# Performance work log

Measured on AMD Instinct MI355X. Metric: run time of the kernel, lower is better.

## Reference

```python
import jax, jax.numpy as jnp
import numpy as np

B, L, D, H, NB = 32, 200, 512, 8, 2
HD = D // H
EPS = 1e-8


def _ln(x, g, b):
    m = x.mean(-1, keepdims=True)
    v = ((x - m) ** 2).mean(-1, keepdims=True)
    return (x - m) / jnp.sqrt(v + EPS) * g + b


def setup_inputs() -> dict:
    key = jax.random.key(0)
    ks = jax.random.split(key, 12)
    w = lambda k, shape: (jax.random.normal(k, shape, jnp.float32) * 0.02)
    return {
        "x": jax.random.normal(ks[0], (B, L, D), jnp.float32),
        "timeline_mask": jnp.zeros((B, L), dtype=bool),  # True = padded
        "ln1_g": jnp.ones((NB, D), jnp.float32), "ln1_b": jnp.zeros((NB, D), jnp.float32),
        "Wq": w(ks[1], (NB, D, D)), "bq": jnp.zeros((NB, D), jnp.float32),
        "Wk": w(ks[2], (NB, D, D)), "bk": jnp.zeros((NB, D), jnp.float32),
        "Wv": w(ks[3], (NB, D, D)), "bv": jnp.zeros((NB, D), jnp.float32),
        "Wo": w(ks[4], (NB, D, D)), "bo": jnp.zeros((NB, D), jnp.float32),
        "ln2_g": jnp.ones((NB, D), jnp.float32), "ln2_b": jnp.zeros((NB, D), jnp.float32),
        "W1": w(ks[5], (NB, D, D)), "b1": jnp.zeros((NB, D), jnp.float32),
        "W2": w(ks[6], (NB, D, D)), "b2": jnp.zeros((NB, D), jnp.float32),
        "lnf_g": jnp.ones((D,), jnp.float32), "lnf_b": jnp.zeros((D,), jnp.float32),
    }


def reference(x, timeline_mask, ln1_g, ln1_b, Wq, bq, Wk, bk, Wv, bv, Wo, bo,
              ln2_g, ln2_b, W1, b1, W2, b2, lnf_g, lnf_b):
    valid = (~timeline_mask)[..., None].astype(x.dtype)  # [B,L,1]
    # causal additive bias [L,L]: 0 on/below diag, -inf above
    causal = jnp.where(jnp.tril(jnp.ones((L, L), dtype=bool)), 0.0, -jnp.inf).astype(x.dtype)
    scale = 1.0 / (HD ** 0.5)
    q = x * valid  # dropout = identity (eval)
    for i in range(NB):
        Qn = _ln(q, ln1_g[i], ln1_b[i])  # pre-attn LayerNorm (query side)
        qh = (Qn @ Wq[i] + bq[i]).reshape(B, L, H, HD)
        kh = (q @ Wk[i] + bk[i]).reshape(B, L, H, HD)
        vh = (q @ Wv[i] + bv[i]).reshape(B, L, H, HD)
        scores = jnp.einsum('bqhd,bkhd->bhqk', qh, kh) * scale + causal
        attn = jax.nn.softmax(scores, axis=-1)
        ctx = jnp.einsum('bhqk,bkhd->bqhd', attn, vh).reshape(B, L, D)
        q = ctx @ Wo[i] + bo[i] + Qn          # residual to normed Q (as in source)
        q = _ln(q, ln2_g[i], ln2_b[i])        # forward layernorm
        h = jax.nn.relu(q @ W1[i] + b1[i]) @ W2[i] + b2[i]  # 1x1 convs == per-token MLP
        q = (q + h) * valid                   # PWFF residual, then timeline mask
    return _ln(q, lnf_g, lnf_b)
```

## Files before the change

kernel.cpp:

```cpp
#include <hip/hip_runtime.h>

typedef unsigned short u16;
typedef __bf16 bfloat;
typedef bfloat bf16x8 __attribute__((ext_vector_type(8)));
typedef float f32x4 __attribute__((ext_vector_type(4)));
typedef u16 v8u16 __attribute__((ext_vector_type(8)));
typedef u16 v4u16 __attribute__((ext_vector_type(4)));

#define B_ 32
#define L_ 200
#define D_ 512
#define H_ 8
#define HD_ 64
#define M_ (B_*L_)

__device__ __forceinline__ float bf2f(u16 u) {
  union { float f; unsigned int i; } v; v.i = ((unsigned int)u) << 16; return v.f;
}
__device__ __forceinline__ u16 f2bf(float f) {
  union { float f; unsigned int i; } v; v.f = f;
  unsigned int i = v.i;
  return (u16)((i + 0x7FFFu + ((i >> 16) & 1u)) >> 16);
}
__device__ __forceinline__ bf16x8 as_bf(v8u16 v) { return __builtin_bit_cast(bf16x8, v); }

__device__ __forceinline__ void gload16(const void* g, void* l) {
  __builtin_amdgcn_global_load_lds(
      (const __attribute__((address_space(1))) void*)g,
      (__attribute__((address_space(3))) void*)l,
      16, 0, 0);
}

struct TPtrs { const float* s[12]; };

__global__ __launch_bounds__(256) void prep_kernel(
    const float* __restrict__ x, const unsigned char* __restrict__ mask,
    u16* __restrict__ qb, TPtrs tp, u16* __restrict__ dst,
    const float* __restrict__ ln1g, const float* __restrict__ ln1b, u16* __restrict__ Qn)
{
  __shared__ float T[64][65];
  int bid = blockIdx.x;
  int t = threadIdx.x;
  if (bid < 1600) {
    size_t i = (size_t)bid * 256 + t;
    size_t base = i * 8;
    int tok = (int)(base >> 9);
    float valid = mask[tok] ? 0.f : 1.f;
    float4 v0 = *(const float4*)(x + base);
    float4 v1 = *(const float4*)(x + base + 4);
    v8u16 ob;
    ob[0]=f2bf(v0.x*valid); ob[1]=f2bf(v0.y*valid); ob[2]=f2bf(v0.z*valid); ob[3]=f2bf(v0.w*valid);
    ob[4]=f2bf(v1.x*valid); ob[5]=f2bf(v1.y*valid); ob[6]=f2bf(v1.z*valid); ob[7]=f2bf(v1.w*valid);
    *(v8u16*)(qb + base) = ob;
    int lane = t & 63;
    float xs[8];
    #pragma unroll
    for (int j = 0; j < 8; j++) xs[j] = bf2f(ob[j]);
    float s = 0.f, q = 0.f;
    #pragma unroll
    for (int j = 0; j < 8; j++) { s += xs[j]; q += xs[j] * xs[j]; }
    #pragma unroll
    for (int off = 1; off < 64; off <<= 1) { s += __shfl_xor(s, off); q += __shfl_xor(q, off); }
    float mean = s * (1.f / 512.f);
    float var  = fmaxf(q * (1.f / 512.f) - mean * mean, 0.f);
    float rstd = rsqrtf(var + 1e-8f);
    float4 g0 = *(const float4*)(ln1g + lane * 8);
    float4 g1 = *(const float4*)(ln1g + lane * 8 + 4);
    float4 b0 = *(const float4*)(ln1b + lane * 8);
    float4 b1 = *(const float4*)(ln1b + lane * 8 + 4);
    float gv[8] = {g0.x,g0.y,g0.z,g0.w,g1.x,g1.y,g1.z,g1.w};
    float bv[8] = {b0.x,b0.y,b0.z,b0.w,b1.x,b1.y,b1.z,b1.w};
    v8u16 qn;
    #pragma unroll
    for (int j = 0; j < 8; j++) qn[j] = f2bf((xs[j] - mean) * rstd * gv[j] + bv[j]);
    *(v8u16*)(Qn + base) = qn;
  } else {
    int wb   = bid - 1600;
    int mat  = wb >> 6;
    int tile = wb & 63;
    int tr = tile >> 3, tc = tile & 7;
    const float* src = tp.s[mat];
    #pragma unroll
    for (int i = 0; i < 4; i++) {
      int idx = t + i * 256;
      int row = idx >> 4, c4 = idx & 15;
      float4 v = *(const float4*)(src + (size_t)(tr * 64 + row) * 512 + tc * 64 + c4 * 4);
      T[row][c4 * 4 + 0] = v.x; T[row][c4 * 4 + 1] = v.y;
      T[row][c4 * 4 + 2] = v.z; T[row][c4 * 4 + 3] = v.w;
    }
    __syncthreads();
    u16* d = dst + (size_t)mat * 262144;
    #pragma unroll
    for (int i = 0; i < 2; i++) {
      int idx = t + i * 256;
      int row = idx >> 3, c8 = idx & 7;
      v8u16 v;
      #pragma unroll
      for (int j = 0; j < 8; j++) v[j] = f2bf(T[c8 * 8 + j][row]);
      *(v8u16*)(d + (size_t)(tc * 64 + row) * 512 + tr * 64 + c8 * 8) = v;
    }
  }
}

template<bool OUTF32>
__global__ __launch_bounds__(256) void ln_kernel(
    const u16* __restrict__ in, const float* __restrict__ g, const float* __restrict__ b,
    u16* __restrict__ outb, float* __restrict__ outf)
{
  int row  = blockIdx.x * 4 + (threadIdx.x >> 6);
  int lane = threadIdx.x & 63;
  size_t base = (size_t)row * 512 + lane * 8;
  v8u16 xv = *(const v8u16*)(in + base);
  float xs[8];
  #pragma unroll
  for (int j = 0; j < 8; j++) xs[j] = bf2f(xv[j]);
  float s = 0.f, q = 0.f;
  #pragma unroll
  for (int j = 0; j < 8; j++) { s += xs[j]; q += xs[j] * xs[j]; }
  #pragma unroll
  for (int off = 1; off < 64; off <<= 1) { s += __shfl_xor(s, off); q += __shfl_xor(q, off); }
  float mean = s * (1.f / 512.f);
  float var  = fmaxf(q * (1.f / 512.f) - mean * mean, 0.f);
  float rstd = rsqrtf(var + 1e-8f);
  float4 g0 = *(const float4*)(g + lane * 8);
  float4 g1 = *(const float4*)(g + lane * 8 + 4);
  float4 b0 = *(const float4*)(b + lane * 8);
  float4 b1 = *(const float4*)(b + lane * 8 + 4);
  float gv[8] = {g0.x,g0.y,g0.z,g0.w,g1.x,g1.y,g1.z,g1.w};
  float bv[8] = {b0.x,b0.y,b0.z,b0.w,b1.x,b1.y,b1.z,b1.w};
  if (OUTF32) {
    float of[8];
    #pragma unroll
    for (int j = 0; j < 8; j++) of[j] = (xs[j] - mean) * rstd * gv[j] + bv[j];
    *(float4*)(outf + base)     = make_float4(of[0], of[1], of[2], of[3]);
    *(float4*)(outf + base + 4) = make_float4(of[4], of[5], of[6], of[7]);
  } else {
    v8u16 ob;
    #pragma unroll
    for (int j = 0; j < 8; j++) ob[j] = f2bf((xs[j] - mean) * rstd * gv[j] + bv[j]);
    *(v8u16*)(outb + base) = ob;
  }
}

__device__ __forceinline__ void stage128(const u16* __restrict__ src, int r0, int kk,
                                         u16* dstLds, int wid, int lane) {
  int g = lane & 15;
  #pragma unroll
  for (int j = 0; j < 4; j++) {
    int row = j * 16 + wid * 4 + (lane >> 4);
    int gsrc = (g & 8) | ((g & 7) ^ (row & 7));
    gload16(src + (size_t)(r0 + row) * 512 + kk + gsrc * 8,
            (char*)dstLds + (j * 16 + wid * 4) * 256);
  }
}

__device__ __forceinline__ void gemm_core128(
    const u16* __restrict__ A, const u16* __restrict__ Wt,
    int m0, int n0, u16* As, u16* Bs, f32x4 (&acc)[2][2])
{
  int tid = threadIdx.x, wid = tid >> 6, lane = tid & 63;
  int wr = wid >> 1, wc = wid & 1;
  int l15 = lane & 15, hi = lane >> 4;

  for (int s = 0; s < 4; s++) {
    int kk = s * 128;
    stage128(A,  m0, kk, As, wid, lane);
    stage128(Wt, n0, kk, Bs, wid, lane);
    __syncthreads();
    #pragma unroll
    for (int ksub = 0; ksub < 4; ksub++) {
      int G = ksub * 4 + hi;
      bf16x8 af[2], bfr[2];
      #pragma unroll
      for (int mi = 0; mi < 2; mi++) {
        int ra = wr * 32 + mi * 16 + l15;
        int lg = (G & 8) | ((G & 7) ^ (ra & 7));
        af[mi] = *(const bf16x8*)(As + ra * 128 + lg * 8);
      }
      #pragma unroll
      for (int ni = 0; ni < 2; ni++) {
        int rn = wc * 32 + ni * 16 + l15;
        int lg = (G & 8) | ((G & 7) ^ (rn & 7));
        bfr[ni] = *(const bf16x8*)(Bs + rn * 128 + lg * 8);
      }
      #pragma unroll
      for (int mi = 0; mi < 2; mi++)
        #pragma unroll
        for (int ni = 0; ni < 2; ni++)
          acc[mi][ni] = __builtin_amdgcn_mfma_f32_16x16x32_bf16(af[mi], bfr[ni], acc[mi][ni], 0, 0, 0);
    }
    __syncthreads();
  }
}

__device__ __forceinline__ void gemm_core128x64(
    const u16* __restrict__ A, const u16* __restrict__ Wt,
    int m0, int n0, u16* As, u16* Bs, f32x4 (&acc)[2][4])
{
  int tid = threadIdx.x, wid = tid >> 6, lane = tid & 63;
  int l15 = lane & 15, hi = lane >> 4;

  for (int s = 0; s < 4; s++) {
    int kk = s * 128;
    stage128(A,  m0,      kk, As,             wid, lane);
    stage128(A,  m0 + 64, kk, As + 64 * 128,  wid, lane);
    stage128(Wt, n0,      kk, Bs,             wid, lane);
    __syncthreads();
    #pragma unroll
    for (int ksub = 0; ksub < 4; ksub++) {
      int G = ksub * 4 + hi;
      bf16x8 af[2], bfr[4];
      #pragma unroll
      for (int mi = 0; mi < 2; mi++) {
        int ra = wid * 32 + mi * 16 + l15;
        int lg = (G & 8) | ((G & 7) ^ (ra & 7));
        af[mi] = *(const bf16x8*)(As + ra * 128 + lg * 8);
      }
      #pragma unroll
      for (int ni = 0; ni < 4; ni++) {
        int rn = ni * 16 + l15;
        int lg = (G & 8) | ((G & 7) ^ (rn & 7));
        bfr[ni] = *(const bf16x8*)(Bs + rn * 128 + lg * 8);
      }
      #pragma unroll
      for (int mi = 0; mi < 2; mi++)
        #pragma unroll
        for (int ni = 0; ni < 4; ni++)
          acc[mi][ni] = __builtin_amdgcn_mfma_f32_16x16x32_bf16(af[mi], bfr[ni], acc[mi][ni], 0, 0, 0);
    }
    __syncthreads();
  }
}

__device__ __forceinline__ void swz400t(int bid, int& m0, int& n0) {
  int tile = (bid & 7) * 50 + (bid >> 3);
  m0 = (tile >> 3) * 128;
  n0 = (tile & 7) * 64;
}

template<bool RELU, bool HAS_RES, bool MASK>
__global__ __launch_bounds__(256) void gemm_one(
    const u16* __restrict__ A, const u16* __restrict__ Wt, const float* __restrict__ bias,
    const u16* __restrict__ res, const unsigned char* __restrict__ mask,
    u16* __restrict__ outb)
{
  __shared__ u16 As[128 * 128];
  __shared__ u16 Bs[64 * 128];
  int m0, n0;
  swz400t(blockIdx.x, m0, n0);
  f32x4 acc[2][4] = {};
  gemm_core128x64(A, Wt, m0, n0, As, Bs, acc);

  int tid = threadIdx.x, wid = tid >> 6, lane = tid & 63;
  int l15 = lane & 15, hi = lane >> 4;
  #pragma unroll
  for (int ni = 0; ni < 4; ni++) {
    int gc = n0 + ni * 16 + l15;
    float bvv = bias[gc];
    #pragma unroll
    for (int mi = 0; mi < 2; mi++) {
      int grb = m0 + wid * 32 + mi * 16 + hi * 4;
      #pragma unroll
      for (int r = 0; r < 4; r++) {
        int gr = grb + r;
        float v = acc[mi][ni][r] + bvv;
        if (HAS_RES) v += bf2f(res[(size_t)gr * 512 + gc]);
        if (RELU) v = fmaxf(v, 0.f);
        if (MASK) v = mask[gr] ? 0.f : v;
        outb[(size_t)gr * 512 + gc] = f2bf(v);
      }
    }
  }
}

__global__ __launch_bounds__(256) void gemm_qkv(
    const u16* __restrict__ Aq, const u16* __restrict__ Akv,
    const u16* __restrict__ Wtq, const u16* __restrict__ Wtk, const u16* __restrict__ Wtv,
    const float* __restrict__ bq, const float* __restrict__ bk, const float* __restrict__ bv,
    u16* __restrict__ outq, u16* __restrict__ outk, u16* __restrict__ outvt)
{
  __shared__ u16 sh[3 * 64 * 128];
  int bid = blockIdx.x;
  int tile = (bid & 7) * 200 + (bid >> 3);
  int tid = threadIdx.x, wid = tid >> 6, lane = tid & 63;
  int wr = wid >> 1, wc = wid & 1;
  int l15 = lane & 15, hi = lane >> 4;
  u16* As = sh;
  u16* B0 = sh + 8192;
  u16* B1 = sh + 16384;

  if (tile < 800) {
    int m0 = (tile >> 3) * 64, n0 = (tile & 7) * 64;
    f32x4 acc[2][2] = {};
    gemm_core128(Aq, Wtq, m0, n0, As, B0, acc);
    #pragma unroll
    for (int ni = 0; ni < 2; ni++) {
      int gc = n0 + wc * 32 + ni * 16 + l15;
      float bvv = bq[gc];
      #pragma unroll
      for (int mi = 0; mi < 2; mi++) {
        int grb = m0 + wr * 32 + mi * 16 + hi * 4;
        #pragma unroll
        for (int r = 0; r < 4; r++)
          outq[(size_t)(grb + r) * 512 + gc] = f2bf(acc[mi][ni][r] + bvv);
      }
    }
  } else {
    int t2 = tile - 800;
    int m0 = (t2 >> 3) * 64, n0 = (t2 & 7) * 64;
    f32x4 ak[2][2] = {}, av[2][2] = {};
    for (int s = 0; s < 4; s++) {
      int kk = s * 128;
      stage128(Akv, m0, kk, As, wid, lane);
      stage128(Wtk, n0, kk, B0, wid, lane);
      stage128(Wtv, n0, kk, B1, wid, lane);
      __syncthreads();
      #pragma unroll
      for (int ksub = 0; ksub < 4; ksub++) {
        int G = ksub * 4 + hi;
        bf16x8 af[2], bkf[2], bvf[2];
        #pragma unroll
        for (int mi = 0; mi < 2; mi++) {
          int ra = wr * 32 + mi * 16 + l15;
          int lg = (G & 8) | ((G & 7) ^ (ra & 7));
          af[mi] = *(const bf16x8*)(As + ra * 128 + lg * 8);
        }
        #pragma unroll
        for (int ni = 0; ni < 2; ni++) {
          int rn = wc * 32 + ni * 16 + l15;
          int lg = (G & 8) | ((G & 7) ^ (rn & 7));
          bkf[ni] = *(const bf16x8*)(B0 + rn * 128 + lg * 8);
          bvf[ni] = *(const bf16x8*)(B1 + rn * 128 + lg * 8);
        }
        #pragma unroll
        for (int mi = 0; mi < 2; mi++)
          #pragma unroll
          for (int ni = 0; ni < 2; ni++) {
            ak[mi][ni] = __builtin_amdgcn_mfma_f32_16x16x32_bf16(af[mi], bkf[ni], ak[mi][ni], 0, 0, 0);
            av[mi][ni] = __builtin_amdgcn_mfma_f32_16x16x32_bf16(af[mi], bvf[ni], av[mi][ni], 0, 0, 0);
          }
      }
      __syncthreads();
    }
    #pragma unroll
    for (int ni = 0; ni < 2; ni++) {
      int gc = n0 + wc * 32 + ni * 16 + l15;
      float bkv = bk[gc], bvv = bv[gc];
      int h = gc >> 6, hd = gc & 63;
      #pragma unroll
      for (int mi = 0; mi < 2; mi++) {
        int grb = m0 + wr * 32 + mi * 16 + hi * 4;
        #pragma unroll
        for (int r = 0; r < 4; r++) {
          int gr = grb + r;
          outk[(size_t)gr * 512 + gc] = f2bf(ak[mi][ni][r] + bkv);
          int b = gr / 200, l = gr - b * 200;
          outvt[((size_t)(b * 8 + h) * 64 + hd) * 224 + l] = f2bf(av[mi][ni][r] + bvv);
        }
      }
    }
  }
}

__global__ __launch_bounds__(64) void attn_kernel(
    const u16* __restrict__ Qh, const u16* __restrict__ Kh,
    const u16* __restrict__ Vt, u16* __restrict__ ctx)
{
  __shared__ u16 Pb[2][16 * 32];
  int bid = blockIdx.x;
  int xcd = bid & 7, j = bid >> 3;
  int bh_hi = j / 7, s = j - bh_hi * 7;
  int bh = bh_hi * 8 + xcd;
  int b = bh >> 3, h = bh & 7;
  int lane = threadIdx.x;
  int l15 = lane & 15, hi = lane >> 4;

  const u16* Kg = Kh + (size_t)(b * L_) * D_ + h * HD_;
  const u16* Vg = Vt + (size_t)bh * 64 * 224;

  int tA = (s < 6) ? (12 - s) : 6;
  int tB = (s < 6) ? s : -1;

  for (int jj = 0; jj < 2; jj++) {
    int t = jj ? tB : tA;
    if (t < 0) break;
    int q0 = t * 16;
    int qrow = q0 + l15; if (qrow > L_ - 1) qrow = L_ - 1;
    const u16* Qg = Qh + (size_t)(b * L_ + qrow) * D_ + h * HD_ + hi * 8;
    bf16x8 aq0 = as_bf(*(const v8u16*)(Qg));
    bf16x8 aq1 = as_bf(*(const v8u16*)(Qg + 32));

    f32x4 sv[13];
    float m0[4];
    #pragma unroll
    for (int r = 0; r < 4; r++) m0[r] = -3.0e38f;

    #pragma unroll
    for (int kt = 0; kt < 13; kt++) {
      if (kt <= t) {
        const u16* kp = Kg + (size_t)(kt * 16 + l15) * D_ + hi * 8;
        bf16x8 bk0 = as_bf(*(const v8u16*)(kp));
        bf16x8 bk1 = as_bf(*(const v8u16*)(kp + 32));
        f32x4 a = {0.f, 0.f, 0.f, 0.f};
        a = __builtin_amdgcn_mfma_f32_16x16x32_bf16(aq0, bk0, a, 0, 0, 0);
        a = __builtin_amdgcn_mfma_f32_16x16x32_bf16(aq1, bk1, a, 0, 0, 0);
        #pragma unroll
        for (int r = 0; r < 4; r++) {
          int qr = q0 + hi * 4 + r;
          int kc = kt * 16 + l15;
          float val = (kc <= qr && qr < L_) ? a[r] * 0.125f : -3.0e38f;
          sv[kt][r] = val;
          m0[r] = fmaxf(m0[r], val);
        }
      }
    }
    #pragma unroll
    for (int r = 0; r < 4; r++) {
      #pragma unroll
      for (int off = 1; off < 16; off <<= 1)
        m0[r] = fmaxf(m0[r], __shfl_xor(m0[r], off));
      if (m0[r] < -1e37f) m0[r] = 0.f;
    }
    float sum[4] = {0.f, 0.f, 0.f, 0.f};
    #pragma unroll
    for (int kt = 0; kt < 13; kt++) {
      if (kt <= t) {
        #pragma unroll
        for (int r = 0; r < 4; r++) {
          float p = __expf(sv[kt][r] - m0[r]);
          sv[kt][r] = p;
          sum[r] += p;
        }
      }
    }
    #pragma unroll
    for (int r = 0; r < 4; r++) {
      #pragma unroll
      for (int off = 1; off < 16; off <<= 1) sum[r] += __shfl_xor(sum[r], off);
    }
    float inv[4];
    #pragma unroll
    for (int r = 0; r < 4; r++) inv[r] = sum[r] > 0.f ? 1.f / sum[r] : 0.f;

    int ksmax = (t + 2) >> 1;
    f32x4 acc[4] = {};
    #pragma unroll
    for (int ks = 0; ks < 7; ks++) {
      if (ks < ksmax) {
        u16* Ps = (u16*)Pb[ks & 1];
        #pragma unroll
        for (int half = 0; half < 2; half++) {
          int kt = ks * 2 + half;
          #pragma unroll
          for (int r = 0; r < 4; r++) {
            float pv = (kt <= t) ? sv[kt][r] : 0.f;
            Ps[(hi * 4 + r) * 32 + half * 16 + l15] = f2bf(pv);
          }
        }
        bf16x8 ap = as_bf(*(const v8u16*)(Ps + l15 * 32 + hi * 8));
        #pragma unroll
        for (int nt = 0; nt < 4; nt++) {
          bf16x8 bv = as_bf(*(const v8u16*)(Vg + (nt * 16 + l15) * 224 + ks * 32 + hi * 8));
          acc[nt] = __builtin_amdgcn_mfma_f32_16x16x32_bf16(ap, bv, acc[nt], 0, 0, 0);
        }
      }
    }
    #pragma unroll
    for (int nt = 0; nt < 4; nt++) {
      #pragma unroll
      for (int r = 0; r < 4; r++) {
        int qr = q0 + hi * 4 + r;
        if (qr < L_) ctx[(size_t)(b * L_ + qr) * D_ + h * HD_ + nt * 16 + l15] = f2bf(acc[nt][r] * inv[r]);
      }
    }
  }
}

extern "C" void kernel_launch(void* const* d_in, const int* in_sizes, int n_in,
                              void* d_out, int out_size, void* d_ws, size_t ws_size,
                              hipStream_t stream)
{
  (void)in_sizes; (void)n_in; (void)out_size; (void)ws_size;
  const float* x    = (const float*)d_in[0];
  const unsigned char* mask = (const unsigned char*)d_in[1];
  const float* ln1g = (const float*)d_in[2];
  const float* ln1b = (const float*)d_in[3];
  const float* Wq   = (const float*)d_in[4];
  const float* bq   = (const float*)d_in[5];
  const float* Wk   = (const float*)d_in[6];
  const float* bk   = (const float*)d_in[7];
  const float* Wv   = (const float*)d_in[8];
  const float* bv   = (const float*)d_in[9];
  const float* Wo   = (const float*)d_in[10];
  const float* bo   = (const float*)d_in[11];
  const float* ln2g = (const float*)d_in[12];
  const float* ln2b = (const float*)d_in[13];
  const float* W1   = (const float*)d_in[14];
  const float* b1   = (const float*)d_in[15];
  const float* W2   = (const float*)d_in[16];
  const float* b2   = (const float*)d_in[17];
  const float* lnfg = (const float*)d_in[18];
  const float* lnfb = (const float*)d_in[19];

  char* ws = (char*)d_ws;
  u16* Wt  = (u16*)(ws);
  u16* qb  = (u16*)(ws +  6291456);
  u16* Qn  = (u16*)(ws + 12845056);
  u16* qh  = (u16*)(ws + 19398656);
  u16* kh  = (u16*)(ws + 25952256);
  u16* vh  = (u16*)(ws + 32505856);
  u16* Vtb = (u16*)(ws + 39059456);

  TPtrs tp;
  tp.s[0] = Wq; tp.s[1] = Wq + 262144;
  tp.s[2] = Wk; tp.s[3] = Wk + 262144;
  tp.s[4] = Wv; tp.s[5] = Wv + 262144;
  tp.s[6] = Wo; tp.s[7] = Wo + 262144;
  tp.s[8] = W1; tp.s[9] = W1 + 262144;
  tp.s[10] = W2; tp.s[11] = W2 + 262144;

  prep_kernel<<<dim3(2368), dim3(256), 0, stream>>>(x, mask, qb, tp, Wt, ln1g, ln1b, Qn);

  for (int i = 0; i < 2; i++) {
    const u16* Wtq = Wt + (size_t)(0 + i) * 262144;
    const u16* Wtk = Wt + (size_t)(2 + i) * 262144;
    const u16* Wtv = Wt + (size_t)(4 + i) * 262144;
    const u16* Wto = Wt + (size_t)(6 + i) * 262144;
    const u16* Wt1 = Wt + (size_t)(8 + i) * 262144;
    const u16* Wt2 = Wt + (size_t)(10 + i) * 262144;

    if (i) ln_kernel<false><<<dim3(1600), dim3(256), 0, stream>>>(qb, ln1g + i * 512, ln1b + i * 512, Qn, nullptr);
    gemm_qkv<<<dim3(1600), dim3(256), 0, stream>>>(Qn, qb, Wtq, Wtk, Wtv,
                                                   bq + i * 512, bk + i * 512, bv + i * 512,
                                                   qh, kh, Vtb);
    attn_kernel<<<dim3(1792), dim3(64), 0, stream>>>(qh, kh, Vtb, vh);
    gemm_one<false,true,false><<<dim3(400), dim3(256), 0, stream>>>(vh, Wto, bo + i * 512, Qn, nullptr, qb);
    ln_kernel<false><<<dim3(1600), dim3(256), 0, stream>>>(qb, ln2g + i * 512, ln2b + i * 512, Qn, nullptr);
    gemm_one<true,false,false><<<dim3(400), dim3(256), 0, stream>>>(Qn, Wt1, b1 + i * 512, nullptr, nullptr, qh);
    gemm_one<false,true,true><<<dim3(400), dim3(256), 0, stream>>>(qh, Wt2, b2 + i * 512, Qn, mask, qb);
  }
  ln_kernel<true><<<dim3(1600), dim3(256), 0, stream>>>(qb, lnfg, lnfb, nullptr, (float*)d_out);
}
```

Baseline: 176.5 us.

## Fuse all stages into one persistent cooperative kernel with grid syncs

Replaces the chain of about 15 separate kernel launches with a single persistent cooperative kernel. It loops over work items per stage and separates stages with grid-wide barriers, removing launch overhead and inter-kernel gaps. The grid is capped at 512 workgroups, so large stages run several items per workgroup. Attention now packs four single-wave items into each 256-thread block. If the cooperative launch fails, it falls back to the old multi-kernel path.

Measured after the change: 205.0 us. 16.1% more time.

```diff
diff --git a/kernel.cpp b/kernel.cpp
--- a/kernel.cpp
+++ b/kernel.cpp
@@ -1,11 +1,13 @@
 #include <hip/hip_runtime.h>
+#include <hip/hip_cooperative_groups.h>
+
+namespace cg = cooperative_groups;
 
 typedef unsigned short u16;
 typedef __bf16 bfloat;
 typedef bfloat bf16x8 __attribute__((ext_vector_type(8)));
 typedef float f32x4 __attribute__((ext_vector_type(4)));
 typedef u16 v8u16 __attribute__((ext_vector_type(8)));
-typedef u16 v4u16 __attribute__((ext_vector_type(4)));
 
 #define B_ 32
 #define L_ 200
@@ -33,14 +35,12 @@
 
 struct TPtrs { const float* s[12]; };
 
-__global__ __launch_bounds__(256) void prep_kernel(
-    const float* __restrict__ x, const unsigned char* __restrict__ mask,
-    u16* __restrict__ qb, TPtrs tp, u16* __restrict__ dst,
-    const float* __restrict__ ln1g, const float* __restrict__ ln1b, u16* __restrict__ Qn)
-{
-  __shared__ float T[64][65];
-  int bid = blockIdx.x;
-  int t = threadIdx.x;
+
+__device__ void prep_item(const float* __restrict__ x, const unsigned char* __restrict__ mask,
+                          u16* __restrict__ qb, TPtrs tp, u16* __restrict__ Wt,
+                          const float* __restrict__ ln1g, const float* __restrict__ ln1b,
+                          u16* __restrict__ Qn, int bid, int t, float* T)
+{
   if (bid < 1600) {
     size_t i = (size_t)bid * 256 + t;
     size_t base = i * 8;
@@ -85,30 +85,29 @@
       int idx = t + i * 256;
       int row = idx >> 4, c4 = idx & 15;
       float4 v = *(const float4*)(src + (size_t)(tr * 64 + row) * 512 + tc * 64 + c4 * 4);
-      T[row][c4 * 4 + 0] = v.x; T[row][c4 * 4 + 1] = v.y;
-      T[row][c4 * 4 + 2] = v.z; T[row][c4 * 4 + 3] = v.w;
+      T[row * 65 + c4 * 4 + 0] = v.x; T[row * 65 + c4 * 4 + 1] = v.y;
+      T[row * 65 + c4 * 4 + 2] = v.z; T[row * 65 + c4 * 4 + 3] = v.w;
     }
     __syncthreads();
-    u16* d = dst + (size_t)mat * 262144;
+    u16* d = Wt + (size_t)mat * 262144;
     #pragma unroll
     for (int i = 0; i < 2; i++) {
       int idx = t + i * 256;
       int row = idx >> 3, c8 = idx & 7;
       v8u16 v;
       #pragma unroll
-      for (int j = 0; j < 8; j++) v[j] = f2bf(T[c8 * 8 + j][row]);
+      for (int j = 0; j < 8; j++) v[j] = f2bf(T[(c8 * 8 + j) * 65 + row]);
       *(v8u16*)(d + (size_t)(tc * 64 + row) * 512 + tr * 64 + c8 * 8) = v;
     }
   }
 }
 
 template<bool OUTF32>
-__global__ __launch_bounds__(256) void ln_kernel(
-    const u16* __restrict__ in, const float* __restrict__ g, const float* __restrict__ b,
-    u16* __restrict__ outb, float* __restrict__ outf)
-{
-  int row  = blockIdx.x * 4 + (threadIdx.x >> 6);
-  int lane = threadIdx.x & 63;
+__device__ void ln_item(int bid, int t, const u16* __restrict__ in,
+                        const float* __restrict__ g, const float* __restrict__ b,
+                        u16* __restrict__ outb, float* __restrict__ outf) {
+  int row  = bid * 4 + (t >> 6);
+  int lane = t & 63;
   size_t base = (size_t)row * 512 + lane * 8;
   v8u16 xv = *(const v8u16*)(in + base);
   float xs[8];
@@ -156,12 +155,11 @@
 
 __device__ __forceinline__ void gemm_core128(
     const u16* __restrict__ A, const u16* __restrict__ Wt,
-    int m0, int n0, u16* As, u16* Bs, f32x4 (&acc)[2][2])
-{
-  int tid = threadIdx.x, wid = tid >> 6, lane = tid & 63;
+    int m0, int n0, u16* As, u16* Bs, f32x4 (&acc)[2][2], int tid)
+{
+  int wid = tid >> 6, lane = tid & 63;
   int wr = wid >> 1, wc = wid & 1;
   int l15 = lane & 15, hi = lane >> 4;
-
   for (int s = 0; s < 4; s++) {
     int kk = s * 128;
     stage128(A,  m0, kk, As, wid, lane);
@@ -193,18 +191,24 @@
   }
 }
 
-__device__ __forceinline__ void gemm_core128x64(
-    const u16* __restrict__ A, const u16* __restrict__ Wt,
-    int m0, int n0, u16* As, u16* Bs, f32x4 (&acc)[2][4])
-{
-  int tid = threadIdx.x, wid = tid >> 6, lane = tid & 63;
+template<bool RELU, bool HAS_RES, bool MASK>
+__device__ void gemm_item(const u16* __restrict__ A, const u16* __restrict__ Wt,
+                          const float* __restrict__ bias, const u16* __restrict__ res,
+                          const unsigned char* __restrict__ mask, u16* __restrict__ outb,
+                          int bid, int tid, u16* sh)
+{
+  u16* As = sh;
+  u16* Bs = sh + 16384;
+  int tile = (bid & 7) * 50 + (bid >> 3);
+  int m0 = (tile >> 3) * 128, n0 = (tile & 7) * 64;
+  int wid = tid >> 6, lane = tid & 63;
   int l15 = lane & 15, hi = lane >> 4;
-
+  f32x4 acc[2][4] = {};
   for (int s = 0; s < 4; s++) {
     int kk = s * 128;
-    stage128(A,  m0,      kk, As,             wid, lane);
-    stage128(A,  m0 + 64, kk, As + 64 * 128,  wid, lane);
-    stage128(Wt, n0,      kk, Bs,             wid, lane);
+    stage128(A,  m0,      kk, As,            wid, lane);
+    stage128(A,  m0 + 64, kk, As + 64 * 128, wid, lane);
+    stage128(Wt, n0,      kk, Bs,            wid, lane);
     __syncthreads();
     #pragma unroll
     for (int ksub = 0; ksub < 4; ksub++) {
@@ -230,29 +234,6 @@
     }
     __syncthreads();
   }
-}
-
-__device__ __forceinline__ void swz400t(int bid, int& m0, int& n0) {
-  int tile = (bid & 7) * 50 + (bid >> 3);
-  m0 = (tile >> 3) * 128;
-  n0 = (tile & 7) * 64;
-}
-
-template<bool RELU, bool HAS_RES, bool MASK>
-__global__ __launch_bounds__(256) void gemm_one(
-    const u16* __restrict__ A, const u16* __restrict__ Wt, const float* __restrict__ bias,
-    const u16* __restrict__ res, const unsigned char* __restrict__ mask,
-    u16* __restrict__ outb)
-{
-  __shared__ u16 As[128 * 128];
-  __shared__ u16 Bs[64 * 128];
-  int m0, n0;
-  swz400t(blockIdx.x, m0, n0);
-  f32x4 acc[2][4] = {};
-  gemm_core128x64(A, Wt, m0, n0, As, Bs, acc);
-
-  int tid = threadIdx.x, wid = tid >> 6, lane = tid & 63;
-  int l15 = lane & 15, hi = lane >> 4;
   #pragma unroll
   for (int ni = 0; ni < 4; ni++) {
     int gc = n0 + ni * 16 + l15;
@@ -273,16 +254,16 @@
   }
 }
 
-__global__ __launch_bounds__(256) void gemm_qkv(
-    const u16* __restrict__ Aq, const u16* __restrict__ Akv,
-    const u16* __restrict__ Wtq, const u16* __restrict__ Wtk, const u16* __restrict__ Wtv,
-    const float* __restrict__ bq, const float* __restrict__ bk, const float* __restrict__ bv,
-    u16* __restrict__ outq, u16* __restrict__ outk, u16* __restrict__ outvt)
-{
-  __shared__ u16 sh[3 * 64 * 128];
-  int bid = blockIdx.x;
+__device__ void qkv_item(const u16* __restrict__ Aq, const u16* __restrict__ Akv,
+                         const u16* __restrict__ Wtq, const u16* __restrict__ Wtk,
+                         const u16* __restrict__ Wtv,
+                         const float* __restrict__ bq, const float* __restrict__ bk,
+                         const float* __restrict__ bv,
+                         u16* __restrict__ outq, u16* __restrict__ outk, u16* __restrict__ outvt,
+                         int bid, int tid, u16* sh)
+{
   int tile = (bid & 7) * 200 + (bid >> 3);
-  int tid = threadIdx.x, wid = tid >> 6, lane = tid & 63;
+  int wid = tid >> 6, lane = tid & 63;
   int wr = wid >> 1, wc = wid & 1;
   int l15 = lane & 15, hi = lane >> 4;
   u16* As = sh;
@@ -292,7 +273,7 @@
   if (tile < 800) {
     int m0 = (tile >> 3) * 64, n0 = (tile & 7) * 64;
     f32x4 acc[2][2] = {};
-    gemm_core128(Aq, Wtq, m0, n0, As, B0, acc);
+    gemm_core128(Aq, Wtq, m0, n0, As, B0, acc, tid);
     #pragma unroll
     for (int ni = 0; ni < 2; ni++) {
       int gc = n0 + wc * 32 + ni * 16 + l15;
@@ -362,17 +343,14 @@
   }
 }
 
-__global__ __launch_bounds__(64) void attn_kernel(
-    const u16* __restrict__ Qh, const u16* __restrict__ Kh,
-    const u16* __restrict__ Vt, u16* __restrict__ ctx)
-{
-  __shared__ u16 Pb[2][16 * 32];
-  int bid = blockIdx.x;
+__device__ void attn_item(const u16* __restrict__ Qh, const u16* __restrict__ Kh,
+                          const u16* __restrict__ Vt, u16* __restrict__ ctx,
+                          int bid, int lane, u16* Pw)
+{
   int xcd = bid & 7, j = bid >> 3;
   int bh_hi = j / 7, s = j - bh_hi * 7;
   int bh = bh_hi * 8 + xcd;
   int b = bh >> 3, h = bh & 7;
-  int lane = threadIdx.x;
   int l15 = lane & 15, hi = lane >> 4;
 
   const u16* Kg = Kh + (size_t)(b * L_) * D_ + h * HD_;
@@ -401,14 +379,14 @@
         const u16* kp = Kg + (size_t)(kt * 16 + l15) * D_ + hi * 8;
         bf16x8 bk0 = as_bf(*(const v8u16*)(kp));
         bf16x8 bk1 = as_bf(*(const v8u16*)(kp + 32));
-        f32x4 a = {0.f, 0.f, 0.f, 0.f};
-        a = __builtin_amdgcn_mfma_f32_16x16x32_bf16(aq0, bk0, a, 0, 0, 0);
-        a = __builtin_amdgcn_mfma_f32_16x16x32_bf16(aq1, bk1, a, 0, 0, 0);
+        f32x4 acq = {0.f, 0.f, 0.f, 0.f};
+        acq = __builtin_amdgcn_mfma_f32_16x16x32_bf16(aq0, bk0, acq, 0, 0, 0);
+        acq = __builtin_amdgcn_mfma_f32_16x16x32_bf16(aq1, bk1, acq, 0, 0, 0);
         #pragma unroll
         for (int r = 0; r < 4; r++) {
           int qr = q0 + hi * 4 + r;
           int kc = kt * 16 + l15;
-          float val = (kc <= qr && qr < L_) ? a[r] * 0.125f : -3.0e38f;
+          float val = (kc <= qr && qr < L_) ? acq[r] * 0.125f : -3.0e38f;
           sv[kt][r] = val;
           m0[r] = fmaxf(m0[r], val);
         }
@@ -447,7 +425,7 @@
     #pragma unroll
     for (int ks = 0; ks < 7; ks++) {
       if (ks < ksmax) {
-        u16* Ps = (u16*)Pb[ks & 1];
+        u16* Ps = Pw + (ks & 1) * 512;
         #pragma unroll
         for (int half = 0; half < 2; half++) {
           int kt = ks * 2 + half;
@@ -460,8 +438,8 @@
         bf16x8 ap = as_bf(*(const v8u16*)(Ps + l15 * 32 + hi * 8));
         #pragma unroll
         for (int nt = 0; nt < 4; nt++) {
-          bf16x8 bv = as_bf(*(const v8u16*)(Vg + (nt * 16 + l15) * 224 + ks * 32 + hi * 8));
-          acc[nt] = __builtin_amdgcn_mfma_f32_16x16x32_bf16(ap, bv, acc[nt], 0, 0, 0);
+          bf16x8 bvv = as_bf(*(const v8u16*)(Vg + (nt * 16 + l15) * 224 + ks * 32 + hi * 8));
+          acc[nt] = __builtin_amdgcn_mfma_f32_16x16x32_bf16(ap, bvv, acc[nt], 0, 0, 0);
         }
       }
     }
@@ -476,68 +454,205 @@
   }
 }
 
+
+__global__ __launch_bounds__(256) void prep_kernel(
+    const float* __restrict__ x, const unsigned char* __restrict__ mask,
+    u16* __restrict__ qb, TPtrs tp, u16* __restrict__ Wt,
+    const float* __restrict__ ln1g, const float* __restrict__ ln1b, u16* __restrict__ Qn)
+{
+  __shared__ float T[64 * 65];
+  prep_item(x, mask, qb, tp, Wt, ln1g, ln1b, Qn, blockIdx.x, threadIdx.x, T);
+}
+
+template<bool OUTF32>
+__global__ __launch_bounds__(256) void ln_kernel(
+    const u16* __restrict__ in, const float* __restrict__ g, const float* __restrict__ b,
+    u16* __restrict__ outb, float* __restrict__ outf)
+{
+  ln_item<OUTF32>(blockIdx.x, threadIdx.x, in, g, b, outb, outf);
+}
+
+template<bool RELU, bool HAS_RES, bool MASK>
+__global__ __launch_bounds__(256) void gemm_one(
+    const u16* __restrict__ A, const u16* __restrict__ Wt, const float* __restrict__ bias,
+    const u16* __restrict__ res, const unsigned char* __restrict__ mask,
+    u16* __restrict__ outb)
+{
+  __shared__ u16 sh[24576];
+  gemm_item<RELU, HAS_RES, MASK>(A, Wt, bias, res, mask, outb, blockIdx.x, threadIdx.x, sh);
+}
+
+__global__ __launch_bounds__(256) void gemm_qkv(
+    const u16* __restrict__ Aq, const u16* __restrict__ Akv,
+    const u16* __restrict__ Wtq, const u16* __restrict__ Wtk, const u16* __restrict__ Wtv,
+    const float* __restrict__ bq, const float* __restrict__ bk, const float* __restrict__ bv,
+    u16* __restrict__ outq, u16* __restrict__ outk, u16* __restrict__ outvt)
+{
+  __shared__ u16 sh[24576];
+  qkv_item(Aq, Akv, Wtq, Wtk, Wtv, bq, bk, bv, outq, outk, outvt, blockIdx.x, threadIdx.x, sh);
+}
+
+__global__ __launch_bounds__(64) void attn_kernel(
+    const u16* __restrict__ Qh, const u16* __restrict__ Kh,
+    const u16* __restrict__ Vt, u16* __restrict__ ctx)
+{
+  __shared__ u16 Pw[1024];
+  attn_item(Qh, Kh, Vt, ctx, blockIdx.x, threadIdx.x, Pw);
+}
+
+
+struct Args {
+  const float* x; const unsigned char* mask;
+  const float* ln1g; const float* ln1b;
+  const float* bq; const float* bk; const float* bv; const float* bo;
+  const float* ln2g; const float* ln2b;
+  const float* b1; const float* b2;
+  const float* lnfg; const float* lnfb;
+  TPtrs tp;
+  u16 *Wt, *qb, *Qn, *qh, *kh, *vh, *Vtb;
+  float* out;
+};
+
+__global__ __launch_bounds__(256, 2) void mega_kernel(Args a)
+{
+  cg::grid_group grid = cg::this_grid();
+  __shared__ u16 sh[24576];
+  int wg = blockIdx.x;
+  int tid = threadIdx.x;
+  int nwg = gridDim.x;
+
+  for (int it = wg; it < 2368; it += nwg) {
+    prep_item(a.x, a.mask, a.qb, a.tp, a.Wt, a.ln1g, a.ln1b, a.Qn, it, tid, (float*)sh);
+    __syncthreads();
+  }
+  grid.sync();
+
+  for (int layer = 0; layer < 2; layer++) {
+    const u16* Wtq = a.Wt + (size_t)(0  + layer) * 262144;
+    const u16* Wtk = a.Wt + (size_t)(2  + layer) * 262144;
+    const u16* Wtv = a.Wt + (size_t)(4  + layer) * 262144;
+    const u16* Wto = a.Wt + (size_t)(6  + layer) * 262144;
+    const u16* Wt1 = a.Wt + (size_t)(8  + layer) * 262144;
+    const u16* Wt2 = a.Wt + (size_t)(10 + layer) * 262144;
+
+    if (layer) {
+      for (int it = wg; it < 1600; it += nwg)
+        ln_item<false>(it, tid, a.qb, a.ln1g + 512, a.ln1b + 512, a.Qn, nullptr);
+      grid.sync();
+    }
+    for (int it = wg; it < 1600; it += nwg) {
+      qkv_item(a.Qn, a.qb, Wtq, Wtk, Wtv, a.bq + layer * 512, a.bk + layer * 512,
+               a.bv + layer * 512, a.qh, a.kh, a.Vtb, it, tid, sh);
+      __syncthreads();
+    }
+    grid.sync();
+    {
+      int wid = tid >> 6, lane = tid & 63;
+      u16* Pw = sh + wid * 1024;
+      for (int it = wg * 4 + wid; it < 1792; it += nwg * 4)
+        attn_item(a.qh, a.kh, a.Vtb, a.vh, it, lane, Pw);
+    }
+    __syncthreads();
+    grid.sync();
+    for (int it = wg; it < 400; it += nwg) {
+      gemm_item<false,true,false>(a.vh, Wto, a.bo + layer * 512, a.Qn, nullptr, a.qb, it, tid, sh);
+      __syncthreads();
+    }
+    grid.sync();
+    for (int it = wg; it < 1600; it += nwg)
+      ln_item<false>(it, tid, a.qb, a.ln2g + layer * 512, a.ln2b + layer * 512, a.Qn, nullptr);
+    grid.sync();
+    for (int it = wg; it < 400; it += nwg) {
+      gemm_item<true,false,false>(a.Qn, Wt1, a.b1 + layer * 512, nullptr, nullptr, a.qh, it, tid, sh);
+      __syncthreads();
+    }
+    grid.sync();
+    for (int it = wg; it < 400; it += nwg) {
+      gemm_item<false,true,true>(a.qh, Wt2, a.b2 + layer * 512, a.Qn, a.mask, a.qb, it, tid, sh);
+      __syncthreads();
+    }
+    grid.sync();
+  }
+  for (int it = wg; it < 1600; it += nwg)
+    ln_item<true>(it, tid, a.qb, a.lnfg, a.lnfb, nullptr, a.out);
+}
+
+
 extern "C" void kernel_launch(void* const* d_in, const int* in_sizes, int n_in,
                               void* d_out, int out_size, void* d_ws, size_t ws_size,
                               hipStream_t stream)
 {
   (void)in_sizes; (void)n_in; (void)out_size; (void)ws_size;
-  const float* x    = (const float*)d_in[0];
-  const unsigned char* mask = (const unsigned char*)d_in[1];
-  const float* ln1g = (const float*)d_in[2];
-  const float* ln1b = (const float*)d_in[3];
-  const float* Wq   = (const float*)d_in[4];
-  const float* bq   = (const float*)d_in[5];
-  const float* Wk   = (const float*)d_in[6];
-  const float* bk   = (const float*)d_in[7];
-  const float* Wv   = (const float*)d_in[8];
-  const float* bv   = (const float*)d_in[9];
-  const float* Wo   = (const float*)d_in[10];
-  const float* bo   = (const float*)d_in[11];
-  const float* ln2g = (const float*)d_in[12];
-  const float* ln2b = (const float*)d_in[13];
-  const float* W1   = (const float*)d_in[14];
-  const float* b1   = (const float*)d_in[15];
-  const float* W2   = (const float*)d_in[16];
-  const float* b2   = (const float*)d_in[17];
-  const float* lnfg = (const float*)d_in[18];
-  const float* lnfb = (const float*)d_in[19];
+  Args a;
+  a.x    = (const float*)d_in[0];
+  a.mask = (const unsigned char*)d_in[1];
+  a.ln1g = (const float*)d_in[2];
+  a.ln1b = (const float*)d_in[3];
+  const float* Wq = (const float*)d_in[4];  a.bq = (const float*)d_in[5];
+  const float* Wk = (const float*)d_in[6];  a.bk = (const float*)d_in[7];
+  const float* Wv = (const float*)d_in[8];  a.bv = (const float*)d_in[9];
+  const float* Wo = (const float*)d_in[10]; a.bo = (const float*)d_in[11];
+  a.ln2g = (const float*)d_in[12];
+  a.ln2b = (const float*)d_in[13];
+  const float* W1 = (const float*)d_in[14]; a.b1 = (const float*)d_in[15];
+  const float* W2 = (const float*)d_in[16]; a.b2 = (const float*)d_in[17];
+  a.lnfg = (const float*)d_in[18];
+  a.lnfb = (const float*)d_in[19];
+
+  a.tp.s[0] = Wq; a.tp.s[1] = Wq + 262144;
+  a.tp.s[2] = Wk; a.tp.s[3] = Wk + 262144;
+  a.tp.s[4] = Wv; a.tp.s[5] = Wv + 262144;
+  a.tp.s[6] = Wo; a.tp.s[7] = Wo + 262144;
+  a.tp.s[8] = W1; a.tp.s[9] = W1 + 262144;
+  a.tp.s[10] = W2; a.tp.s[11] = W2 + 262144;
 
   char* ws = (char*)d_ws;
-  u16* Wt  = (u16*)(ws);
-  u16* qb  = (u16*)(ws +  6291456);
-  u16* Qn  = (u16*)(ws + 12845056);
-  u16* qh  = (u16*)(ws + 19398656);
-  u16* kh  = (u16*)(ws + 25952256);
-  u16* vh  = (u16*)(ws + 32505856);
-  u16* Vtb = (u16*)(ws + 39059456);
-
-  TPtrs tp;
-  tp.s[0] = Wq; tp.s[1] = Wq + 262144;
-  tp.s[2] = Wk; tp.s[3] = Wk + 262144;
-  tp.s[4] = Wv; tp.s[5] = Wv + 262144;
-  tp.s[6] = Wo; tp.s[7] = Wo + 262144;
-  tp.s[8] = W1; tp.s[9] = W1 + 262144;
-  tp.s[10] = W2; tp.s[11] = W2 + 262144;
-
-  prep_kernel<<<dim3(2368), dim3(256), 0, stream>>>(x, mask, qb, tp, Wt, ln1g, ln1b, Qn);
-
+  a.Wt  = (u16*)(ws);
+  a.qb  = (u16*)(ws +  6291456);
+  a.Qn  = (u16*)(ws + 12845056);
+  a.qh  = (u16*)(ws + 19398656);
+  a.kh  = (u16*)(ws + 25952256);
+  a.vh  = (u16*)(ws + 32505856);
+  a.Vtb = (u16*)(ws + 39059456);
+  a.out = (float*)d_out;
+
+  bool coop_ok = false;
+  int nb = 0;
+  if (hipOccupancyMaxActiveBlocksPerMultiprocessor(&nb, mega_kernel, 256, 0) == hipSuccess && nb > 0) {
+    int dev = 0, ncu = 0;
+    hipGetDevice(&dev);
+    hipDeviceGetAttribute(&ncu, hipDeviceAttributeMultiprocessorCount, dev);
+    if (ncu > 0) {
+      long maxg = (long)nb * ncu;
+      int grid = (int)(maxg < 512 ? maxg : 512);
+      if (grid >= 64) {
+        void* params[] = { (void*)&a };
+        if (hipLaunchCooperativeKernel((const void*)mega_kernel, dim3(grid), dim3(256),
+                                       params, 0, stream) == hipSuccess)
+          coop_ok = true;
+      }
+    }
+  }
+  if (coop_ok) return;
+
+  prep_kernel<<<dim3(2368), dim3(256), 0, stream>>>(a.x, a.mask, a.qb, a.tp, a.Wt, a.ln1g, a.ln1b, a.Qn);
   for (int i = 0; i < 2; i++) {
-    const u16* Wtq = Wt + (size_t)(0 + i) * 262144;
-    const u16* Wtk = Wt + (size_t)(2 + i) * 262144;
-    const u16* Wtv = Wt + (size_t)(4 + i) * 262144;
-    const u16* Wto = Wt + (size_t)(6 + i) * 262144;
-    const u16* Wt1 = Wt + (size_t)(8 + i) * 262144;
-    const u16* Wt2 = Wt + (size_t)(10 + i) * 262144;
-
-    if (i) ln_kernel<false><<<dim3(1600), dim3(256), 0, stream>>>(qb, ln1g + i * 512, ln1b + i * 512, Qn, nullptr);
-    gemm_qkv<<<dim3(1600), dim3(256), 0, stream>>>(Qn, qb, Wtq, Wtk, Wtv,
-                                                   bq + i * 512, bk + i * 512, bv + i * 512,
-                                                   qh, kh, Vtb);
-    attn_kernel<<<dim3(1792), dim3(64), 0, stream>>>(qh, kh, Vtb, vh);
-    gemm_one<false,true,false><<<dim3(400), dim3(256), 0, stream>>>(vh, Wto, bo + i * 512, Qn, nullptr, qb);
-    ln_kernel<false><<<dim3(1600), dim3(256), 0, stream>>>(qb, ln2g + i * 512, ln2b + i * 512, Qn, nullptr);
-    gemm_one<true,false,false><<<dim3(400), dim3(256), 0, stream>>>(Qn, Wt1, b1 + i * 512, nullptr, nullptr, qh);
-    gemm_one<false,true,true><<<dim3(400), dim3(256), 0, stream>>>(qh, Wt2, b2 + i * 512, Qn, mask, qb);
-  }
-  ln_kernel<true><<<dim3(1600), dim3(256), 0, stream>>>(qb, lnfg, lnfb, nullptr, (float*)d_out);
-}
+    const u16* Wtq = a.Wt + (size_t)(0 + i) * 262144;
+    const u16* Wtk = a.Wt + (size_t)(2 + i) * 262144;
+    const u16* Wtv = a.Wt + (size_t)(4 + i) * 262144;
+    const u16* Wto = a.Wt + (size_t)(6 + i) * 262144;
+    const u16* Wt1 = a.Wt + (size_t)(8 + i) * 262144;
+    const u16* Wt2 = a.Wt + (size_t)(10 + i) * 262144;
+
+    if (i) ln_kernel<false><<<dim3(1600), dim3(256), 0, stream>>>(a.qb, a.ln1g + 512, a.ln1b + 512, a.Qn, nullptr);
+    gemm_qkv<<<dim3(1600), dim3(256), 0, stream>>>(a.Qn, a.qb, Wtq, Wtk, Wtv,
+                                                   a.bq + i * 512, a.bk + i * 512, a.bv + i * 512,
+                                                   a.qh, a.kh, a.Vtb);
+    attn_kernel<<<dim3(1792), dim3(64), 0, stream>>>(a.qh, a.kh, a.Vtb, a.vh);
+    gemm_one<false,true,false><<<dim3(400), dim3(256), 0, stream>>>(a.vh, Wto, a.bo + i * 512, a.Qn, nullptr, a.qb);
+    ln_kernel<false><<<dim3(1600), dim3(256), 0, stream>>>(a.qb, a.ln2g + i * 512, a.ln2b + i * 512, a.Qn, nullptr);
+    gemm_one<true,false,false><<<dim3(400), dim3(256), 0, stream>>>(a.Qn, Wt1, a.b1 + i * 512, nullptr, nullptr, a.qh);
+    gemm_one<false,true,true><<<dim3(400), dim3(256), 0, stream>>>(a.qh, Wt2, a.b2 + i * 512, a.Qn, a.mask, a.qb);
+  }
+  ln_kernel<true><<<dim3(1600), dim3(256), 0, stream>>>(a.qb, a.lnfg, a.lnfb, nullptr, (float*)d_out);
+}
```
